# Optimization experiments

Measured on AMD Instinct MI355X. Metric: run time of the kernel, lower is better.

The kernel has to match this reference:

```python
import jax, jax.numpy as jnp
import numpy as np
from jax import lax

B, CIN, COUT, K = 32, 32, 32, 3
H = W = 128
COND_DIM = 256
NUM_PARAMS = CIN * COUT * K * K      # 9216
HIDDEN = NUM_PARAMS // 2             # 4608
STRIDE, PAD = 1, 1


def setup_inputs() -> dict:
    key = jax.random.key(0)
    ks = jax.random.split(key, 6)
    return {
        "x": jax.random.normal(ks[0], (B, CIN, H, W), dtype=jnp.float32),
        "cond": jax.random.normal(ks[1], (B, COND_DIM), dtype=jnp.float32),
        "W1": jax.random.normal(ks[2], (HIDDEN, COND_DIM), dtype=jnp.float32) * 0.02,
        "b1": jax.random.normal(ks[3], (HIDDEN,), dtype=jnp.float32) * 0.02,
        "W2": jax.random.normal(ks[4], (NUM_PARAMS, HIDDEN), dtype=jnp.float32) * 0.02,
        "b2": jax.random.normal(ks[5], (NUM_PARAMS,), dtype=jnp.float32) * 0.02,
    }


def reference(x, cond, W1, b1, W2, b2):
    # Hypernetwork MLP: cond [B, cond_dim] -> per-sample conv weights
    h = jax.nn.relu(jnp.einsum('bc,hc->bh', cond, W1) + b1)      # [B, HIDDEN]
    w = jnp.einsum('bh,ph->bp', h, W2) + b2                      # [B, NUM_PARAMS]
    w = w.reshape(B * COUT, CIN, K, K)                           # [B*Cout, Cin, K, K]

    # Per-sample conv2d fused as a single grouped conv (groups = B):
    # fold batch into channels of a single example.
    lhs = x.reshape(1, B * CIN, H, W)
    out = lax.conv_general_dilated(
        lhs, w,
        window_strides=(STRIDE, STRIDE),
        padding=[(PAD, PAD), (PAD, PAD)],
        dimension_numbers=('NCHW', 'OIHW', 'NCHW'),
        feature_group_count=B,
    )  # [1, B*Cout, H', W']
    return out.reshape(B, COUT, out.shape[2], out.shape[3])
```

## Files before the change

### kernel.cpp

```cpp
#include <hip/hip_runtime.h>
#include <cstdint>
#include <cstddef>

#define B_    32
#define CIN_  32
#define COUT_ 32
#define HH    128
#define WW    128
#define CDIM  256
#define NP    9216
#define HID   4608
#define KSPLIT 4
#define KPER  (HID/KSPLIT)

__global__ __launch_bounds__(256)
void mlp1_k(const float* __restrict__ cond, const float* __restrict__ W1,
            const float* __restrict__ b1, float* __restrict__ h) {
    __shared__ float cs[CDIM];
    const int b  = blockIdx.x / (HID/256);
    const int jb = blockIdx.x % (HID/256);
    const int tid = threadIdx.x;
    cs[tid] = cond[b*CDIM + tid];
    __syncthreads();
    const int j = jb*256 + tid;
    const float4* wr = reinterpret_cast<const float4*>(W1 + (size_t)j*CDIM);
    float acc = b1[j];
    #pragma unroll 4
    for (int c = 0; c < CDIM/4; ++c) {
        float4 w = wr[c];
        acc += w.x*cs[4*c] + w.y*cs[4*c+1] + w.z*cs[4*c+2] + w.w*cs[4*c+3];
    }
    h[b*HID + j] = fmaxf(acc, 0.f);
}

__global__ __launch_bounds__(256)
void mlp2_k(const float* __restrict__ h, const float* __restrict__ W2,
            float* __restrict__ part) {
    __shared__ float hs[B_*68];
    __shared__ float w2s[64*68];
    const int pblk = blockIdx.x >> 2;
    const int ks   = blockIdx.x & 3;
    const int p0   = pblk * 64;
    const int tid  = threadIdx.x;
    const int pl   = tid & 63;
    const int bg   = tid >> 6;
    float acc[8] = {0,0,0,0,0,0,0,0};
    const int kbase0 = ks * KPER;
    for (int kt = 0; kt < KPER/64; ++kt) {
        const int kb = kbase0 + kt*64;
        __syncthreads();
        for (int i = tid; i < B_*64; i += 256) {
            int bb = i >> 6, kk = i & 63;
            hs[bb*68 + kk] = h[bb*HID + kb + kk];
        }
        for (int q = tid; q < 64*16; q += 256) {
            int pp = q >> 4, kq = (q & 15) << 2;
            float4 v = *reinterpret_cast<const float4*>(W2 + (size_t)(p0+pp)*HID + kb + kq);
            *reinterpret_cast<float4*>(&w2s[pp*68 + kq]) = v;
        }
        __syncthreads();
        #pragma unroll 4
        for (int k4 = 0; k4 < 16; ++k4) {
            float4 wv = *reinterpret_cast<const float4*>(&w2s[pl*68 + k4*4]);
            #pragma unroll
            for (int i = 0; i < 8; ++i) {
                float4 hv = *reinterpret_cast<const float4*>(&hs[(bg*8+i)*68 + k4*4]);
                acc[i] += wv.x*hv.x + wv.y*hv.y + wv.z*hv.z + wv.w*hv.w;
            }
        }
    }
    float* dst = part + (size_t)ks*B_*NP;
    #pragma unroll
    for (int i = 0; i < 8; ++i)
        dst[(size_t)(bg*8+i)*NP + p0 + pl] = acc[i];
}

__global__ __launch_bounds__(256)
void reduce_k(const float* __restrict__ part, const float* __restrict__ b2,
              float* __restrict__ wt) {
    const int idx = blockIdx.x*256 + threadIdx.x;
    const float4* p4 = reinterpret_cast<const float4*>(part);
    const size_t stride = (size_t)B_*NP/4;
    float4 a = p4[idx];
    float4 b = p4[idx + stride];
    float4 c = p4[idx + 2*stride];
    float4 d = p4[idx + 3*stride];
    const int pq = idx % (NP/4);
    const int bi = idx / (NP/4);
    float4 bb = reinterpret_cast<const float4*>(b2)[pq];
    float o0 = a.x+b.x+c.x+d.x+bb.x;
    float o1 = a.y+b.y+c.y+d.y+bb.y;
    float o2 = a.z+b.z+c.z+d.z+bb.z;
    float o3 = a.w+b.w+c.w+d.w+bb.w;
    const int p  = pq << 2;
    const int co = p / 288;
    const int r  = p - co*288;
    float* dst = wt + (size_t)bi*NP + r*32 + co;
    dst[0]  = o0;
    dst[32] = o1;
    dst[64] = o2;
    dst[96] = o3;
}

#define CG 8
__global__ __launch_bounds__(256, 4)
void conv_k(const float* __restrict__ x, const float* __restrict__ wt,
            float* __restrict__ out) {
    __shared__ float xs[CG*6*132];
    __shared__ float wsh[CG*9*32];
    const int b   = blockIdx.x >> 5;
    const int r0  = (blockIdx.x & 31) << 2;
    const int tid = threadIdx.x;
    const int colb = tid & 15;
    const int cg   = (tid >> 4) & 7;
    const int rp   = tid >> 7;
    const int col8 = colb << 3;
    float acc[2][4][8] = {};
    for (int g = 0; g < 4; ++g) {
        const int c0 = g * CG;
        __syncthreads();
        for (int i = tid; i < CG*6*132; i += 256) {
            int ci  = i / 792;
            int rem = i - ci*792;
            int rr  = rem / 132;
            int cp  = rem - rr*132;
            int gr  = r0 - 1 + rr;
            int gc  = cp - 1;
            float v = 0.f;
            if ((unsigned)gr < HH && (unsigned)gc < WW)
                v = x[(((size_t)b*CIN_ + c0 + ci)*HH + gr)*WW + gc];
            xs[i] = v;
        }
        {
            const float4* src4 = reinterpret_cast<const float4*>(
                wt + (size_t)b*NP + c0*9*32);
            float4* dst4 = reinterpret_cast<float4*>(wsh);
            for (int q = tid; q < CG*9*32/4; q += 256)
                dst4[q] = src4[q];
        }
        __syncthreads();
        for (int ci = 0; ci < CG; ++ci) {
            #pragma unroll
            for (int t = 0; t < 4; ++t) {
                float xrow[12];
                {
                    const float4* p4 = reinterpret_cast<const float4*>(
                        &xs[(ci*6 + 2*rp + t)*132 + col8]);
                    float4 q0 = p4[0], q1 = p4[1], q2 = p4[2];
                    xrow[0]=q0.x; xrow[1]=q0.y; xrow[2] =q0.z; xrow[3] =q0.w;
                    xrow[4]=q1.x; xrow[5]=q1.y; xrow[6] =q1.z; xrow[7] =q1.w;
                    xrow[8]=q2.x; xrow[9]=q2.y; xrow[10]=q2.z; xrow[11]=q2.w;
                }
                #pragma unroll
                for (int kh = 0; kh < 3; ++kh) {
                    const int ro = t - kh;
                    if (ro < 0 || ro > 1) continue;
                    #pragma unroll
                    for (int kw = 0; kw < 3; ++kw) {
                        const float4 w4 = *reinterpret_cast<const float4*>(
                            &wsh[(ci*9 + kh*3 + kw)*32 + cg*4]);
                        #pragma unroll
                        for (int cl = 0; cl < 8; ++cl) {
                            const float xv = xrow[cl + kw];
                            acc[ro][0][cl] = fmaf(xv, w4.x, acc[ro][0][cl]);
                            acc[ro][1][cl] = fmaf(xv, w4.y, acc[ro][1][cl]);
                            acc[ro][2][cl] = fmaf(xv, w4.z, acc[ro][2][cl]);
                            acc[ro][3][cl] = fmaf(xv, w4.w, acc[ro][3][cl]);
                        }
                    }
                }
            }
        }
    }
    #pragma unroll
    for (int ro = 0; ro < 2; ++ro) {
        const int row = r0 + 2*rp + ro;
        #pragma unroll
        for (int c = 0; c < 4; ++c) {
            const int cout = cg*4 + c;
            float* dst = out + (((size_t)b*COUT_ + cout)*HH + row)*WW + col8;
            *reinterpret_cast<float4*>(dst) =
                make_float4(acc[ro][c][0], acc[ro][c][1], acc[ro][c][2], acc[ro][c][3]);
            *reinterpret_cast<float4*>(dst + 4) =
                make_float4(acc[ro][c][4], acc[ro][c][5], acc[ro][c][6], acc[ro][c][7]);
        }
    }
}

extern "C" void kernel_launch(void* const* d_in, const int* in_sizes, int n_in,
                              void* d_out, int out_size, void* d_ws, size_t ws_size,
                              hipStream_t stream) {
    const float* x    = (const float*)d_in[0];
    const float* cond = (const float*)d_in[1];
    const float* W1   = (const float*)d_in[2];
    const float* b1   = (const float*)d_in[3];
    const float* W2   = (const float*)d_in[4];
    const float* b2   = (const float*)d_in[5];
    float* out = (float*)d_out;

    char* ws = (char*)d_ws;
    float* h    = (float*)(ws);
    float* part = (float*)(ws + 589824);
    float* wt   = (float*)(ws + 589824 + 4718592);

    hipLaunchKernelGGL(mlp1_k,   dim3(B_*(HID/256)),    dim3(256), 0, stream, cond, W1, b1, h);
    hipLaunchKernelGGL(mlp2_k,   dim3((NP/64)*KSPLIT),  dim3(256), 0, stream, h, W2, part);
    hipLaunchKernelGGL(reduce_k, dim3((B_*NP/4)/256),   dim3(256), 0, stream, part, b2, wt);
    hipLaunchKernelGGL(conv_k,   dim3(B_*(HH/4)),       dim3(256), 0, stream, x, wt, out);
}
```

Before: 558.2 us.

## Rewrite hypernet GEMM as register-blocked per-thread rows and pad conv smem

The second MLP layer is restructured so each thread owns one output parameter row and accumulates all 32 batch entries in registers. It streams W2 directly from global memory, reads a transposed hidden activation through uniform broadcast loads, and splits K eight ways instead of four. The conv kernel gets a padded shared-memory row layout with coalesced per-warp loads, and hoists its nine weight float4 loads out of the inner loop. The aim is to cut shared-memory traffic and bank conflicts, at the cost of higher register pressure and a larger partial-sum buffer for the reduce step.

```diff
diff --git a/kernel.cpp b/kernel.cpp
--- a/kernel.cpp
+++ b/kernel.cpp
@@ -10,12 +10,12 @@
 #define CDIM  256
 #define NP    9216
 #define HID   4608
-#define KSPLIT 4
-#define KPER  (HID/KSPLIT)
+#define KS2   8
+#define KPER2 (HID/KS2)
 
 __global__ __launch_bounds__(256)
 void mlp1_k(const float* __restrict__ cond, const float* __restrict__ W1,
-            const float* __restrict__ b1, float* __restrict__ h) {
+            const float* __restrict__ b1, float* __restrict__ ht) {
     __shared__ float cs[CDIM];
     const int b  = blockIdx.x / (HID/256);
     const int jb = blockIdx.x % (HID/256);
@@ -30,49 +30,38 @@
         float4 w = wr[c];
         acc += w.x*cs[4*c] + w.y*cs[4*c+1] + w.z*cs[4*c+2] + w.w*cs[4*c+3];
     }
-    h[b*HID + j] = fmaxf(acc, 0.f);
-}
-
-__global__ __launch_bounds__(256)
-void mlp2_k(const float* __restrict__ h, const float* __restrict__ W2,
+    ht[(size_t)j*B_ + b] = fmaxf(acc, 0.f);
+}
+
+__global__ __launch_bounds__(64)
+void mlp2_k(const float* __restrict__ ht, const float* __restrict__ W2,
             float* __restrict__ part) {
-    __shared__ float hs[B_*68];
-    __shared__ float w2s[64*68];
-    const int pblk = blockIdx.x >> 2;
-    const int ks   = blockIdx.x & 3;
-    const int p0   = pblk * 64;
-    const int tid  = threadIdx.x;
-    const int pl   = tid & 63;
-    const int bg   = tid >> 6;
-    float acc[8] = {0,0,0,0,0,0,0,0};
-    const int kbase0 = ks * KPER;
-    for (int kt = 0; kt < KPER/64; ++kt) {
-        const int kb = kbase0 + kt*64;
-        __syncthreads();
-        for (int i = tid; i < B_*64; i += 256) {
-            int bb = i >> 6, kk = i & 63;
-            hs[bb*68 + kk] = h[bb*HID + kb + kk];
-        }
-        for (int q = tid; q < 64*16; q += 256) {
-            int pp = q >> 4, kq = (q & 15) << 2;
-            float4 v = *reinterpret_cast<const float4*>(W2 + (size_t)(p0+pp)*HID + kb + kq);
-            *reinterpret_cast<float4*>(&w2s[pp*68 + kq]) = v;
-        }
-        __syncthreads();
-        #pragma unroll 4
-        for (int k4 = 0; k4 < 16; ++k4) {
-            float4 wv = *reinterpret_cast<const float4*>(&w2s[pl*68 + k4*4]);
-            #pragma unroll
-            for (int i = 0; i < 8; ++i) {
-                float4 hv = *reinterpret_cast<const float4*>(&hs[(bg*8+i)*68 + k4*4]);
-                acc[i] += wv.x*hv.x + wv.y*hv.y + wv.z*hv.z + wv.w*hv.w;
-            }
-        }
-    }
-    float* dst = part + (size_t)ks*B_*NP;
-    #pragma unroll
-    for (int i = 0; i < 8; ++i)
-        dst[(size_t)(bg*8+i)*NP + p0 + pl] = acc[i];
+    const int pblk = blockIdx.x >> 3;
+    const int ks   = blockIdx.x & 7;
+    const int p    = pblk*64 + threadIdx.x;
+    const int k0   = ks * KPER2;
+    const float* w2row = W2 + (size_t)p*HID + k0;
+    const float* hrow  = ht + (size_t)k0*B_;
+    float acc[B_];
+    #pragma unroll
+    for (int b = 0; b < B_; ++b) acc[b] = 0.f;
+    float hA[B_], hB[B_];
+    #pragma unroll
+    for (int b = 0; b < B_; ++b) hA[b] = hrow[b];
+    for (int k = 0; k < KPER2; k += 2) {
+        const float2 wv = *reinterpret_cast<const float2*>(w2row + k);
+        #pragma unroll
+        for (int b = 0; b < B_; ++b) hB[b] = hrow[(k+1)*B_ + b];
+        #pragma unroll
+        for (int b = 0; b < B_; ++b) acc[b] = fmaf(hA[b], wv.x, acc[b]);
+        #pragma unroll
+        for (int b = 0; b < B_; ++b) hA[b] = hrow[(k+2)*B_ + b];
+        #pragma unroll
+        for (int b = 0; b < B_; ++b) acc[b] = fmaf(hB[b], wv.y, acc[b]);
+    }
+    float* dst = part + (size_t)ks*B_*NP + p;
+    #pragma unroll
+    for (int b = 0; b < B_; ++b) dst[(size_t)b*NP] = acc[b];
 }
 
 __global__ __launch_bounds__(256)
@@ -81,17 +70,15 @@
     const int idx = blockIdx.x*256 + threadIdx.x;
     const float4* p4 = reinterpret_cast<const float4*>(part);
     const size_t stride = (size_t)B_*NP/4;
-    float4 a = p4[idx];
-    float4 b = p4[idx + stride];
-    float4 c = p4[idx + 2*stride];
-    float4 d = p4[idx + 3*stride];
     const int pq = idx % (NP/4);
     const int bi = idx / (NP/4);
     float4 bb = reinterpret_cast<const float4*>(b2)[pq];
-    float o0 = a.x+b.x+c.x+d.x+bb.x;
-    float o1 = a.y+b.y+c.y+d.y+bb.y;
-    float o2 = a.z+b.z+c.z+d.z+bb.z;
-    float o3 = a.w+b.w+c.w+d.w+bb.w;
+    float o0 = bb.x, o1 = bb.y, o2 = bb.z, o3 = bb.w;
+    #pragma unroll
+    for (int s = 0; s < KS2; ++s) {
+        float4 v = p4[idx + (size_t)s*stride];
+        o0 += v.x; o1 += v.y; o2 += v.z; o3 += v.w;
+    }
     const int p  = pq << 2;
     const int co = p / 288;
     const int r  = p - co*288;
@@ -103,10 +90,11 @@
 }
 
 #define CG 8
+#define XROW 148
 __global__ __launch_bounds__(256, 4)
 void conv_k(const float* __restrict__ x, const float* __restrict__ wt,
             float* __restrict__ out) {
-    __shared__ float xs[CG*6*132];
+    __shared__ float xs[CG*6*XROW];
     __shared__ float wsh[CG*9*32];
     const int b   = blockIdx.x >> 5;
     const int r0  = (blockIdx.x & 31) << 2;
@@ -115,21 +103,32 @@
     const int cg   = (tid >> 4) & 7;
     const int rp   = tid >> 7;
     const int col8 = colb << 3;
+    const int po0 = col8     + 4*((col8)    >> 5);
+    const int po1 = col8 + 4 + 4*((col8+4) >> 5);
+    const int po2 = col8 + 8 + 4*((col8+8) >> 5);
+    const int lane32 = tid & 31;
+    const int ci_s   = tid >> 5;
     float acc[2][4][8] = {};
     for (int g = 0; g < 4; ++g) {
         const int c0 = g * CG;
         __syncthreads();
-        for (int i = tid; i < CG*6*132; i += 256) {
-            int ci  = i / 792;
-            int rem = i - ci*792;
-            int rr  = rem / 132;
-            int cp  = rem - rr*132;
-            int gr  = r0 - 1 + rr;
-            int gc  = cp - 1;
-            float v = 0.f;
-            if ((unsigned)gr < HH && (unsigned)gc < WW)
-                v = x[(((size_t)b*CIN_ + c0 + ci)*HH + gr)*WW + gc];
-            xs[i] = v;
+        {
+            const float* xc = x + ((size_t)b*CIN_ + c0 + ci_s)*HH*WW;
+            for (int rr = 0; rr < 6; ++rr) {
+                const int gr = r0 - 1 + rr;
+                const int rok = ((unsigned)gr < HH);
+                const float* xrowp = xc + (size_t)gr*WW - 1;
+                float* xsrow = xs + (ci_s*6 + rr)*XROW;
+                #pragma unroll
+                for (int s = 0; s < 5; ++s) {
+                    const int cp = s*32 + lane32;
+                    if (s == 4 && lane32 >= 4) continue;
+                    const int gc = cp - 1;
+                    float v = 0.f;
+                    if (rok && (unsigned)gc < WW) v = xrowp[cp];
+                    xsrow[cp + s*4] = v;
+                }
+            }
         }
         {
             const float4* src4 = reinterpret_cast<const float4*>(
@@ -140,13 +139,19 @@
         }
         __syncthreads();
         for (int ci = 0; ci < CG; ++ci) {
+            float4 wv[9];
+            #pragma unroll
+            for (int k9 = 0; k9 < 9; ++k9)
+                wv[k9] = *reinterpret_cast<const float4*>(
+                    &wsh[(ci*9 + k9)*32 + cg*4]);
             #pragma unroll
             for (int t = 0; t < 4; ++t) {
                 float xrow[12];
                 {
-                    const float4* p4 = reinterpret_cast<const float4*>(
-                        &xs[(ci*6 + 2*rp + t)*132 + col8]);
-                    float4 q0 = p4[0], q1 = p4[1], q2 = p4[2];
+                    const float* xbase = xs + (ci*6 + 2*rp + t)*XROW;
+                    float4 q0 = *reinterpret_cast<const float4*>(xbase + po0);
+                    float4 q1 = *reinterpret_cast<const float4*>(xbase + po1);
+                    float4 q2 = *reinterpret_cast<const float4*>(xbase + po2);
                     xrow[0]=q0.x; xrow[1]=q0.y; xrow[2] =q0.z; xrow[3] =q0.w;
                     xrow[4]=q1.x; xrow[5]=q1.y; xrow[6] =q1.z; xrow[7] =q1.w;
                     xrow[8]=q2.x; xrow[9]=q2.y; xrow[10]=q2.z; xrow[11]=q2.w;
@@ -157,8 +162,7 @@
                     if (ro < 0 || ro > 1) continue;
                     #pragma unroll
                     for (int kw = 0; kw < 3; ++kw) {
-                        const float4 w4 = *reinterpret_cast<const float4*>(
-                            &wsh[(ci*9 + kh*3 + kw)*32 + cg*4]);
+                        const float4 w4 = wv[kh*3 + kw];
                         #pragma unroll
                         for (int cl = 0; cl < 8; ++cl) {
                             const float xv = xrow[cl + kw];
@@ -199,12 +203,12 @@
     float* out = (float*)d_out;
 
     char* ws = (char*)d_ws;
-    float* h    = (float*)(ws);
-    float* part = (float*)(ws + 589824);
-    float* wt   = (float*)(ws + 589824 + 4718592);
-
-    hipLaunchKernelGGL(mlp1_k,   dim3(B_*(HID/256)),    dim3(256), 0, stream, cond, W1, b1, h);
-    hipLaunchKernelGGL(mlp2_k,   dim3((NP/64)*KSPLIT),  dim3(256), 0, stream, h, W2, part);
-    hipLaunchKernelGGL(reduce_k, dim3((B_*NP/4)/256),   dim3(256), 0, stream, part, b2, wt);
-    hipLaunchKernelGGL(conv_k,   dim3(B_*(HH/4)),       dim3(256), 0, stream, x, wt, out);
-}
+    float* ht   = (float*)(ws);
+    float* part = (float*)(ws + 590080);
+    float* wt   = (float*)(ws + 590080 + 9437184);
+
+    hipLaunchKernelGGL(mlp1_k,   dim3(B_*(HID/256)),   dim3(256), 0, stream, cond, W1, b1, ht);
+    hipLaunchKernelGGL(mlp2_k,   dim3((NP/64)*KS2),    dim3(64),  0, stream, ht, W2, part);
+    hipLaunchKernelGGL(reduce_k, dim3((B_*NP/4)/256),  dim3(256), 0, stream, part, b2, wt);
+    hipLaunchKernelGGL(conv_k,   dim3(B_*(HH/4)),      dim3(256), 0, stream, x, wt, out);
+}
```

After: 620.5 us. +11.2%, slower.
